# Performance work log

Hardware: AMD Instinct MI355X
Metric: run time of the kernel (lower is better)

## Reference

```python
import jax, jax.numpy as jnp
import numpy as np

NEG_SLOPE = 0.01  # torch F.leaky_relu default
NUM_USER, NUM_ITEM, DIM = 50000, 30000, 64
N_NODES = NUM_USER + NUM_ITEM
N_INTER = 800000
N_LAYERS = 2


def _leaky(x):
    return jax.nn.leaky_relu(x, NEG_SLOPE)


def _gcn_tower(features, preference, id_embedding, W, b, row, col):
    # x = cat(preference, features); F.normalize (L2 per row)
    x = jnp.concatenate([preference, features], axis=0)  # [N, 64]
    x = x / jnp.maximum(jnp.linalg.norm(x, axis=1, keepdims=True), 1e-12)
    deg = jax.ops.segment_sum(jnp.ones(row.shape, x.dtype), row, num_segments=N_NODES)  # bincount(row)
    for i in range(N_LAYERS):
        # Abstract_GCN: scatter-mean of gathered neighbor feats, then linear
        agg = jax.ops.segment_sum(x[col], row, num_segments=N_NODES) / deg[:, None]
        h = _leaky(agg @ W[i, 0].T + b[i, 0])
        # has_id=True, concate=False
        x_hat = _leaky(x @ W[i, 1].T + b[i, 1]) + id_embedding
        x = _leaky(h @ W[i, 2].T + b[i, 2] + x_hat)
    return x


def setup_inputs() -> dict:
    key = jax.random.key(0)
    ks = jax.random.split(key, 14)
    # bipartite user->item edges with full node coverage (every node appears
    # as a row after symmetrization, matching real interaction data where
    # bincount(row) has no zeros)
    r1 = jnp.arange(NUM_USER, dtype=jnp.int64 if jax.config.jax_enable_x64 else jnp.int32)
    c1 = jax.random.randint(ks[0], (NUM_USER,), NUM_USER, N_NODES)
    r2 = jax.random.randint(ks[1], (NUM_ITEM,), 0, NUM_USER)
    c2 = NUM_USER + jnp.arange(NUM_ITEM, dtype=r1.dtype)
    rest = N_INTER - NUM_USER - NUM_ITEM
    r3 = jax.random.randint(ks[2], (rest,), 0, NUM_USER)
    c3 = jax.random.randint(ks[3], (rest,), NUM_USER, N_NODES)
    row0 = jnp.concatenate([r1, r2, r3])
    col0 = jnp.concatenate([c1, c2, c3])
    # symmetrize: cat(edge_index, edge_index[[1,0]])
    edge_index = jnp.stack([jnp.concatenate([row0, col0]),
                            jnp.concatenate([col0, row0])])  # [2, 1.6M]
    s = 0.1  # xavier-ish scale for 64x64
    return {
        "v_feat": jax.random.normal(ks[4], (NUM_ITEM, DIM), jnp.float32),
        "t_feat": jax.random.normal(ks[5], (NUM_ITEM, DIM), jnp.float32),
        "id_embedding": jax.random.normal(ks[6], (N_NODES, DIM), jnp.float32) * s,
        "v_pref": jax.random.normal(ks[7], (NUM_USER, DIM), jnp.float32) * s,
        "t_pref": jax.random.normal(ks[8], (NUM_USER, DIM), jnp.float32) * s,
        "v_W": jax.random.normal(ks[9], (N_LAYERS, 3, DIM, DIM), jnp.float32) * s,
        "v_b": jnp.zeros((N_LAYERS, 3, DIM), jnp.float32),
        "t_W": jax.random.normal(ks[10], (N_LAYERS, 3, DIM, DIM), jnp.float32) * s,
        "t_b": jnp.zeros((N_LAYERS, 3, DIM), jnp.float32),
        "edge_index": edge_index,
    }


def reference(v_feat, t_feat, id_embedding, v_pref, t_pref, v_W, v_b, t_W, t_b, edge_index):
    row, col = edge_index[0], edge_index[1]
    rep_v = _gcn_tower(v_feat, v_pref, id_embedding, v_W, v_b, row, col)
    rep_t = _gcn_tower(t_feat, t_pref, id_embedding, t_W, t_b, row, col)
    return (rep_v + rep_t) / 2.0  # MMGCN.get_rep representation
```

## Files before the change

kernel.cpp:

```cpp
#include <hip/hip_runtime.h>
#include <hip/hip_bf16.h>

#define NUM_USER 50000
#define N_NODES  80000
#define DIM      64
#define NEG_SLOPE 0.01f

#define NB 313
#define BSHIFT 8
#define RMASK 255
#define CSHIFT 17
#define CMASK 0x1FFFF
#define CAP 10240

typedef __attribute__((ext_vector_type(8))) short short8;
typedef __attribute__((ext_vector_type(4))) float f32x4;

typedef unsigned short XT;

__device__ __forceinline__ float leaky(float v) {
    return v > 0.0f ? v : v * NEG_SLOPE;
}

__device__ __forceinline__ int load_idx(const void* ei, int is64, long long pos) {
    if (is64) return (int)((const long long*)ei)[pos];
    return ((const int*)ei)[pos];
}
__device__ __forceinline__ float load_f(const void* p, int isbf16, size_t i) {
    if (isbf16) return __bfloat162float(((const __hip_bfloat16*)p)[i]);
    return ((const float*)p)[i];
}

__device__ __forceinline__ unsigned short f2bf(float f) {
    unsigned u = __float_as_uint(f);
    u += 0x7fffu + ((u >> 16) & 1u);
    return (unsigned short)(u >> 16);
}

__device__ __forceinline__ void acc8(float* a, uint4 r) {
    a[0] += __uint_as_float(r.x << 16);
    a[1] += __uint_as_float(r.x & 0xffff0000u);
    a[2] += __uint_as_float(r.y << 16);
    a[3] += __uint_as_float(r.y & 0xffff0000u);
    a[4] += __uint_as_float(r.z << 16);
    a[5] += __uint_as_float(r.z & 0xffff0000u);
    a[6] += __uint_as_float(r.w << 16);
    a[7] += __uint_as_float(r.w & 0xffff0000u);
}

__global__ void detect_kernel(const unsigned int* __restrict__ feat_words,
                              const int* __restrict__ ei_words,
                              int* __restrict__ flags,
                              int* __restrict__ bucketCur) {
    int lane = threadIdx.x & 63;
    for (int i = lane; i < 320; i += 64) bucketCur[i] = 0;
    int orv = 0;
    for (int i = lane * 2 + 1; i < 1024; i += 128) orv |= ei_words[i];
    int hits = 0;
    for (int i = lane; i < 256; i += 64) {
        unsigned e = (feat_words[i] >> 7) & 0xFF;
        hits += (e == 126 || e == 127) ? 1 : 0;
    }
    #pragma unroll
    for (int d = 32; d > 0; d >>= 1) {
        orv  |= __shfl_xor(orv, d, 64);
        hits += __shfl_xor(hits, d, 64);
    }
    if (lane == 0 && blockIdx.x == 0) {
        flags[0] = (orv == 0) ? 1 : 0;
        flags[1] = (hits > 64) ? 1 : 0;
    }
}

__global__ __launch_bounds__(256) void megafuse_kernel(
        const void* __restrict__ ei, int E, int binBlocks, int initBlocks,
        const int* __restrict__ flags,
        int* __restrict__ bucketCur, unsigned int* __restrict__ recs,
        const void* __restrict__ vp, const void* __restrict__ tp,
        const void* __restrict__ vf, const void* __restrict__ tf,
        XT* __restrict__ xc,
        const void* __restrict__ vW, const void* __restrict__ tW,
        const void* __restrict__ vb, const void* __restrict__ tb,
        unsigned short* __restrict__ Wbf, float* __restrict__ bfp) {
    if ((int)blockIdx.x < binBlocks) {
        __shared__ int bloc[320];
        __shared__ int bres[320];
        int tid = threadIdx.x;
        for (int i = tid; i < 320; i += 256) bloc[i] = 0;
        __syncthreads();
        int is64 = flags[0];
        long long base = (long long)blockIdx.x * 2048;
        int bb[8], cc[8], lp[8], rl[8];
        #pragma unroll
        for (int it = 0; it < 8; ++it) {
            bb[it] = -1;
            long long e = base + it * 256 + tid;
            if (e < E) {
                int r = load_idx(ei, is64, e);
                int c = load_idx(ei, is64, (long long)E + e);
                if ((unsigned)r < N_NODES && (unsigned)c < N_NODES) {
                    int b = r >> BSHIFT;
                    bb[it] = b;
                    cc[it] = c;
                    rl[it] = r & RMASK;
                    lp[it] = atomicAdd(&bloc[b], 1);
                }
            }
        }
        __syncthreads();
        for (int i = tid; i < NB; i += 256) {
            int v = bloc[i];
            bres[i] = v ? atomicAdd(&bucketCur[i], v) : 0;
        }
        __syncthreads();
        #pragma unroll
        for (int it = 0; it < 8; ++it) {
            if (bb[it] >= 0) {
                int pos = bres[bb[it]] + lp[it];
                if (pos < CAP)
                    recs[(size_t)bb[it] * CAP + pos] =
                        ((unsigned)rl[it] << CSHIFT) | (unsigned)cc[it];
            }
        }
    } else if ((int)blockIdx.x < binBlocks + initBlocks) {
        int n = (blockIdx.x - binBlocks) * 4 + (threadIdx.x >> 6);
        if (n >= N_NODES) return;
        int lane = threadIdx.x & 63;
        int isb = flags[1];
        float a, b;
        if (n < NUM_USER) {
            a = load_f(vp, isb, (size_t)n * DIM + lane);
            b = load_f(tp, isb, (size_t)n * DIM + lane);
        } else {
            a = load_f(vf, isb, (size_t)(n - NUM_USER) * DIM + lane);
            b = load_f(tf, isb, (size_t)(n - NUM_USER) * DIM + lane);
        }
        float sa = a * a, sb = b * b;
        #pragma unroll
        for (int d = 32; d > 0; d >>= 1) {
            sa += __shfl_xor(sa, d, 64);
            sb += __shfl_xor(sb, d, 64);
        }
        float ra = 1.0f / fmaxf(sqrtf(sa), 1e-12f);
        float rb = 1.0f / fmaxf(sqrtf(sb), 1e-12f);
        xc[(size_t)n * 128 + lane]      = f2bf(a * ra);
        xc[(size_t)n * 128 + 64 + lane] = f2bf(b * rb);
    } else {
        int isb = flags[1];
        int j = (blockIdx.x - binBlocks - initBlocks) * 256 + threadIdx.x;
        if (j < 2 * 24576) {
            int tw = j / 24576, r = j % 24576;
            Wbf[j] = f2bf(load_f(tw ? tW : vW, isb, r));
        } else if (j < 2 * 24576 + 2 * 384) {
            int i2 = j - 2 * 24576;
            int tw = i2 / 384, r = i2 % 384;
            bfp[i2] = load_f(tw ? tb : vb, isb, r);
        }
    }
}

__global__ __launch_bounds__(1024) void bin2csr_kernel(
        const unsigned int* __restrict__ recs,
        const int* __restrict__ bucketCur,
        int* __restrict__ cnt, int* __restrict__ cur,
        int* __restrict__ csr) {
    __shared__ int rcnt[256];
    __shared__ int sc[256];
    __shared__ int lcur[256];
    int b = blockIdx.x;
    int t = threadIdx.x;
    int base = b * CAP;
    int count = bucketCur[b];
    if (count > CAP) count = CAP;

    if (t < 256) { rcnt[t] = 0; lcur[t] = 0; }
    __syncthreads();
    for (int i = t; i < count; i += 1024) {
        unsigned rec = recs[(size_t)base + i];
        atomicAdd(&rcnt[rec >> CSHIFT], 1);
    }
    __syncthreads();
    int v = (t < 256) ? rcnt[t] : 0;
    if (t < 256) sc[t] = v;
    __syncthreads();
    for (int d = 1; d < 256; d <<= 1) {
        int x = 0;
        if (t < 256) { x = sc[t]; if (t >= d) x += sc[t - d]; }
        __syncthreads();
        if (t < 256) sc[t] = x;
        __syncthreads();
    }
    if (t < 256) {
        int row = (b << BSHIFT) + t;
        if (row < N_NODES) {
            cnt[row] = v;
            cur[row] = base + sc[t];
        }
    }
    __syncthreads();
    for (int i = t; i < count; i += 1024) {
        unsigned rec = recs[(size_t)base + i];
        int rloc = rec >> CSHIFT;
        int c = rec & CMASK;
        int pos = base + (sc[rloc] - rcnt[rloc]) + atomicAdd(&lcur[rloc], 1);
        csr[pos] = c;
    }
}

__global__ __launch_bounds__(512) void gather_kernel(
        const XT* __restrict__ xc, XT* __restrict__ agg,
        const int* __restrict__ cnt, const int* __restrict__ cur,
        const int* __restrict__ csr) {
    int n = blockIdx.x * 8 + (threadIdx.x >> 6);
    if (n >= N_NODES) return;
    int lane = threadIdx.x & 63;
    int g8 = lane >> 3;
    int s  = lane & 7;
    int gg = g8 >> 1;
    int h  = g8 & 1;

    int d = cnt[n];
    int base = cur[n] - d;
    const int* nb = csr + base;
    const XT* xh = xc + h * 64;

    float acc[8];
    #pragma unroll
    for (int f = 0; f < 8; ++f) acc[f] = 0.f;

    int jj = gg;
    for (; jj + 4 < d; jj += 8) {
        int c0 = nb[jj];
        int c1 = nb[jj + 4];
        uint4 r0 = ((const uint4*)(xh + (size_t)c0 * 128))[s];
        uint4 r1 = ((const uint4*)(xh + (size_t)c1 * 128))[s];
        acc8(acc, r0);
        acc8(acc, r1);
    }
    if (jj < d) {
        int c0 = nb[jj];
        uint4 r0 = ((const uint4*)(xh + (size_t)c0 * 128))[s];
        acc8(acc, r0);
    }

    #pragma unroll
    for (int dd = 16; dd < 64; dd <<= 1) {
        #pragma unroll
        for (int f = 0; f < 8; ++f) acc[f] += __shfl_xor(acc[f], dd, 64);
    }

    float invd = (d > 0) ? 1.0f / (float)d : 0.0f;
    if (g8 < 2) {
        uint4 w;
        w.x = (unsigned)f2bf(acc[0] * invd) | ((unsigned)f2bf(acc[1] * invd) << 16);
        w.y = (unsigned)f2bf(acc[2] * invd) | ((unsigned)f2bf(acc[3] * invd) << 16);
        w.z = (unsigned)f2bf(acc[4] * invd) | ((unsigned)f2bf(acc[5] * invd) << 16);
        w.w = (unsigned)f2bf(acc[6] * invd) | ((unsigned)f2bf(acc[7] * invd) << 16);
        ((uint4*)(agg + (size_t)n * 128 + h * 64))[s] = w;
    }
}

__global__ __launch_bounds__(512) void dense_mfma_kernel(
        XT* __restrict__ xc, const XT* __restrict__ agg,
        const void* __restrict__ id_emb,
        const unsigned short* __restrict__ Wbf, const float* __restrict__ bfp,
        int layer, const int* __restrict__ flags) {
    __shared__ unsigned short Wl[3 * 64 * 72];
    __shared__ unsigned short hts[8][16 * 72];
    int tower = blockIdx.y;
    int wave = threadIdx.x >> 6, lane = threadIdx.x & 63;
    int quad = lane >> 4, l16 = lane & 15;
    int isb = flags[1];
    int toff = tower * 64;
    const unsigned short* Wg = Wbf + (size_t)((tower * 2 + layer) * 3) * 4096;
    const float* bb = bfp + (tower * 2 + layer) * 192;
    unsigned short* ht = hts[wave];

    for (int i = threadIdx.x; i < 1536; i += 512) {
        int lin = i * 8;
        int mat = lin >> 12;
        int rem = lin & 4095;
        uint4 v = *(const uint4*)(Wg + lin);
        *(uint4*)(Wl + mat * 4608 + (rem >> 6) * 72 + (rem & 63)) = v;
    }
    __syncthreads();

    int n0 = (blockIdx.x * 8 + wave) * 16;
    size_t arow = (size_t)(n0 + l16) * 128 + toff + quad * 8;

    short8 x0  = *(const short8*)(xc + arow);
    short8 x1  = *(const short8*)(xc + arow + 32);
    short8 ga0 = *(const short8*)(agg + arow);
    short8 ga1 = *(const short8*)(agg + arow + 32);

    f32x4 accP[4];

    #pragma unroll
    for (int t = 0; t < 4; ++t) {
        f32x4 c = {0.f, 0.f, 0.f, 0.f};
        short8 b0 = *(const short8*)(Wl + 4608 + (16 * t + l16) * 72 + quad * 8);
        short8 b1 = *(const short8*)(Wl + 4608 + (16 * t + l16) * 72 + 32 + quad * 8);
        c = __builtin_amdgcn_mfma_f32_16x16x32_bf16(x0, b0, c, 0, 0, 0);
        c = __builtin_amdgcn_mfma_f32_16x16x32_bf16(x1, b1, c, 0, 0, 0);
        float bias = bb[64 + 16 * t + l16];
        #pragma unroll
        for (int r = 0; r < 4; ++r) accP[t][r] = leaky(c[r] + bias);
    }

    #pragma unroll
    for (int t = 0; t < 4; ++t) {
        f32x4 c = {0.f, 0.f, 0.f, 0.f};
        short8 b0 = *(const short8*)(Wl + (16 * t + l16) * 72 + quad * 8);
        short8 b1 = *(const short8*)(Wl + (16 * t + l16) * 72 + 32 + quad * 8);
        c = __builtin_amdgcn_mfma_f32_16x16x32_bf16(ga0, b0, c, 0, 0, 0);
        c = __builtin_amdgcn_mfma_f32_16x16x32_bf16(ga1, b1, c, 0, 0, 0);
        float bias = bb[16 * t + l16];
        #pragma unroll
        for (int r = 0; r < 4; ++r)
            ht[(quad * 4 + r) * 72 + 16 * t + l16] = f2bf(leaky(c[r] + bias));
    }

    float idv[16];
    #pragma unroll
    for (int t = 0; t < 4; ++t)
        #pragma unroll
        for (int r = 0; r < 4; ++r)
            idv[t * 4 + r] = load_f(id_emb, isb,
                                    (size_t)(n0 + quad * 4 + r) * 64 + 16 * t + l16);

    short8 a0 = *(const short8*)(ht + l16 * 72 + quad * 8);
    short8 a1 = *(const short8*)(ht + l16 * 72 + 32 + quad * 8);

    #pragma unroll
    for (int t = 0; t < 4; ++t) {
        f32x4 c = {0.f, 0.f, 0.f, 0.f};
        short8 b0 = *(const short8*)(Wl + 2 * 4608 + (16 * t + l16) * 72 + quad * 8);
        short8 b1 = *(const short8*)(Wl + 2 * 4608 + (16 * t + l16) * 72 + 32 + quad * 8);
        c = __builtin_amdgcn_mfma_f32_16x16x32_bf16(a0, b0, c, 0, 0, 0);
        c = __builtin_amdgcn_mfma_f32_16x16x32_bf16(a1, b1, c, 0, 0, 0);
        float bias = bb[128 + 16 * t + l16];
        #pragma unroll
        for (int r = 0; r < 4; ++r) {
            int node2 = n0 + quad * 4 + r;
            int j = 16 * t + l16;
            float v = leaky(c[r] + bias + accP[t][r] + idv[t * 4 + r]);
            xc[(size_t)node2 * 128 + toff + j] = f2bf(v);
        }
    }
}

__global__ void final_kernel(const XT* __restrict__ xc, void* __restrict__ out,
                             const int* __restrict__ flags, int n8) {
    int i = blockIdx.x * blockDim.x + threadIdx.x;
    if (i >= n8) return;
    int n = i >> 3, s = i & 7;
    uint4 v = ((const uint4*)(xc + (size_t)n * 128))[s];
    uint4 t = ((const uint4*)(xc + (size_t)n * 128 + 64))[s];
    float r[8];
    r[0] = (__uint_as_float(v.x << 16) + __uint_as_float(t.x << 16)) * 0.5f;
    r[1] = (__uint_as_float(v.x & 0xffff0000u) + __uint_as_float(t.x & 0xffff0000u)) * 0.5f;
    r[2] = (__uint_as_float(v.y << 16) + __uint_as_float(t.y << 16)) * 0.5f;
    r[3] = (__uint_as_float(v.y & 0xffff0000u) + __uint_as_float(t.y & 0xffff0000u)) * 0.5f;
    r[4] = (__uint_as_float(v.z << 16) + __uint_as_float(t.z << 16)) * 0.5f;
    r[5] = (__uint_as_float(v.z & 0xffff0000u) + __uint_as_float(t.z & 0xffff0000u)) * 0.5f;
    r[6] = (__uint_as_float(v.w << 16) + __uint_as_float(t.w << 16)) * 0.5f;
    r[7] = (__uint_as_float(v.w & 0xffff0000u) + __uint_as_float(t.w & 0xffff0000u)) * 0.5f;
    if (flags[1]) {
        uint4 o;
        o.x = (unsigned)f2bf(r[0]) | ((unsigned)f2bf(r[1]) << 16);
        o.y = (unsigned)f2bf(r[2]) | ((unsigned)f2bf(r[3]) << 16);
        o.z = (unsigned)f2bf(r[4]) | ((unsigned)f2bf(r[5]) << 16);
        o.w = (unsigned)f2bf(r[6]) | ((unsigned)f2bf(r[7]) << 16);
        ((uint4*)out)[i] = o;
    } else {
        float4* o = (float4*)out;
        o[i * 2 + 0] = make_float4(r[0], r[1], r[2], r[3]);
        o[i * 2 + 1] = make_float4(r[4], r[5], r[6], r[7]);
    }
}

extern "C" void kernel_launch(void* const* d_in, const int* in_sizes, int n_in,
                              void* d_out, int out_size, void* d_ws, size_t ws_size,
                              hipStream_t stream) {
    const void* v_feat = d_in[0];
    const void* t_feat = d_in[1];
    const void* id_emb = d_in[2];
    const void* v_pref = d_in[3];
    const void* t_pref = d_in[4];
    const void* v_W    = d_in[5];
    const void* v_b    = d_in[6];
    const void* t_W    = d_in[7];
    const void* t_b    = d_in[8];
    const void* ei     = d_in[9];

    const int E = in_sizes[9] / 2;
    char* ws = (char*)d_ws;

    size_t o = 0;
    int*            flags     = (int*)(ws + o);            o += 16;
    int*            cnt       = (int*)(ws + o);            o += 320000;
    int*            cur       = (int*)(ws + o);            o += 320000;
    int*            bucketCur = (int*)(ws + o);            o += 320 * 4;
    unsigned short* Wbf       = (unsigned short*)(ws + o); o += 2 * 24576 * 2;
    float*          bfp       = (float*)(ws + o);          o += 2 * 384 * 4;
    XT* xc  = (XT*)(ws + o); o += (size_t)N_NODES * 128 * sizeof(XT);
    XT* agg = (XT*)(ws + o); o += (size_t)N_NODES * 128 * sizeof(XT);
    unsigned int* recs = (unsigned int*)(ws + o); o += (size_t)NB * CAP * 4;
    int* csr = (int*)(ws + o);

    detect_kernel<<<dim3(1), dim3(64), 0, stream>>>(
        (const unsigned int*)v_feat, (const int*)ei, flags, bucketCur);

    const int binBlocks  = (E + 2047) / 2048;
    const int initBlocks = (N_NODES + 3) / 4;
    const int packBlocks = (2 * 24576 + 2 * 384 + 255) / 256;
    megafuse_kernel<<<dim3(binBlocks + initBlocks + packBlocks), dim3(256), 0, stream>>>(
        ei, E, binBlocks, initBlocks, flags, bucketCur, recs,
        v_pref, t_pref, v_feat, t_feat, xc,
        v_W, t_W, v_b, t_b, Wbf, bfp);

    bin2csr_kernel<<<dim3(NB), dim3(1024), 0, stream>>>(recs, bucketCur, cnt, cur, csr);

    const int gatherBlocks = (N_NODES + 7) / 8;
    const int denseBlocksX = N_NODES / (16 * 8);

    for (int layer = 0; layer < 2; ++layer) {
        gather_kernel<<<dim3(gatherBlocks), dim3(512), 0, stream>>>(xc, agg, cnt, cur, csr);
        dense_mfma_kernel<<<dim3(denseBlocksX, 2), dim3(512), 0, stream>>>(
            xc, agg, id_emb, Wbf, bfp, layer, flags);
    }

    const int n8 = N_NODES * DIM / 8;
    final_kernel<<<dim3((n8 + 255) / 256), dim3(256), 0, stream>>>(xc, d_out, flags, n8);
}
```

Measured before the change: 344.6 us.

## Split interleaved tower feature buffers into separate per-tower arrays

After: 354.6 us. 2.9% more time.

```diff
diff --git a/kernel.cpp b/kernel.cpp
--- a/kernel.cpp
+++ b/kernel.cpp
@@ -78,7 +78,7 @@
         int* __restrict__ bucketCur, unsigned int* __restrict__ recs,
         const void* __restrict__ vp, const void* __restrict__ tp,
         const void* __restrict__ vf, const void* __restrict__ tf,
-        XT* __restrict__ xc,
+        XT* __restrict__ xv, XT* __restrict__ xt,
         const void* __restrict__ vW, const void* __restrict__ tW,
         const void* __restrict__ vb, const void* __restrict__ tb,
         unsigned short* __restrict__ Wbf, float* __restrict__ bfp) {
@@ -143,8 +143,8 @@
         }
         float ra = 1.0f / fmaxf(sqrtf(sa), 1e-12f);
         float rb = 1.0f / fmaxf(sqrtf(sb), 1e-12f);
-        xc[(size_t)n * 128 + lane]      = f2bf(a * ra);
-        xc[(size_t)n * 128 + 64 + lane] = f2bf(b * rb);
+        xv[(size_t)n * 64 + lane] = f2bf(a * ra);
+        xt[(size_t)n * 64 + lane] = f2bf(b * rb);
     } else {
         int isb = flags[1];
         int j = (blockIdx.x - binBlocks - initBlocks) * 256 + threadIdx.x;
@@ -208,70 +208,73 @@
 }
 
 __global__ __launch_bounds__(512) void gather_kernel(
-        const XT* __restrict__ xc, XT* __restrict__ agg,
+        const XT* __restrict__ xv, const XT* __restrict__ xt,
+        XT* __restrict__ aggv, XT* __restrict__ aggt,
         const int* __restrict__ cnt, const int* __restrict__ cur,
         const int* __restrict__ csr) {
     int n = blockIdx.x * 8 + (threadIdx.x >> 6);
     if (n >= N_NODES) return;
+    int tower = blockIdx.y;
+    const XT* xh = tower ? xt : xv;
+    XT* ah = tower ? aggt : aggv;
     int lane = threadIdx.x & 63;
-    int g8 = lane >> 3;
-    int s  = lane & 7;
-    int gg = g8 >> 1;
-    int h  = g8 & 1;
+    int g = lane >> 3;
+    int s = lane & 7;
 
     int d = cnt[n];
     int base = cur[n] - d;
     const int* nb = csr + base;
-    const XT* xh = xc + h * 64;
 
     float acc[8];
     #pragma unroll
     for (int f = 0; f < 8; ++f) acc[f] = 0.f;
 
-    int jj = gg;
-    for (; jj + 4 < d; jj += 8) {
+    int jj = g;
+    for (; jj + 8 < d; jj += 16) {
         int c0 = nb[jj];
-        int c1 = nb[jj + 4];
-        uint4 r0 = ((const uint4*)(xh + (size_t)c0 * 128))[s];
-        uint4 r1 = ((const uint4*)(xh + (size_t)c1 * 128))[s];
+        int c1 = nb[jj + 8];
+        uint4 r0 = ((const uint4*)(xh + (size_t)c0 * 64))[s];
+        uint4 r1 = ((const uint4*)(xh + (size_t)c1 * 64))[s];
         acc8(acc, r0);
         acc8(acc, r1);
     }
     if (jj < d) {
         int c0 = nb[jj];
-        uint4 r0 = ((const uint4*)(xh + (size_t)c0 * 128))[s];
+        uint4 r0 = ((const uint4*)(xh + (size_t)c0 * 64))[s];
         acc8(acc, r0);
     }
 
     #pragma unroll
-    for (int dd = 16; dd < 64; dd <<= 1) {
+    for (int dd = 8; dd < 64; dd <<= 1) {
         #pragma unroll
         for (int f = 0; f < 8; ++f) acc[f] += __shfl_xor(acc[f], dd, 64);
     }
 
     float invd = (d > 0) ? 1.0f / (float)d : 0.0f;
-    if (g8 < 2) {
+    if (g == 0) {
         uint4 w;
         w.x = (unsigned)f2bf(acc[0] * invd) | ((unsigned)f2bf(acc[1] * invd) << 16);
         w.y = (unsigned)f2bf(acc[2] * invd) | ((unsigned)f2bf(acc[3] * invd) << 16);
         w.z = (unsigned)f2bf(acc[4] * invd) | ((unsigned)f2bf(acc[5] * invd) << 16);
         w.w = (unsigned)f2bf(acc[6] * invd) | ((unsigned)f2bf(acc[7] * invd) << 16);
-        ((uint4*)(agg + (size_t)n * 128 + h * 64))[s] = w;
+        ((uint4*)(ah + (size_t)n * 64))[s] = w;
     }
 }
 
 __global__ __launch_bounds__(512) void dense_mfma_kernel(
-        XT* __restrict__ xc, const XT* __restrict__ agg,
+        XT* __restrict__ xv, XT* __restrict__ xt,
+        const XT* __restrict__ aggv, const XT* __restrict__ aggt,
         const void* __restrict__ id_emb,
         const unsigned short* __restrict__ Wbf, const float* __restrict__ bfp,
         int layer, const int* __restrict__ flags) {
     __shared__ unsigned short Wl[3 * 64 * 72];
     __shared__ unsigned short hts[8][16 * 72];
     int tower = blockIdx.y;
+    XT* xh = tower ? xt : xv;
+    const XT* ah = tower ? aggt : aggv;
     int wave = threadIdx.x >> 6, lane = threadIdx.x & 63;
     int quad = lane >> 4, l16 = lane & 15;
     int isb = flags[1];
-    int toff = tower * 64;
     const unsigned short* Wg = Wbf + (size_t)((tower * 2 + layer) * 3) * 4096;
     const float* bb = bfp + (tower * 2 + layer) * 192;
     unsigned short* ht = hts[wave];
@@ -286,12 +289,12 @@
     __syncthreads();
 
     int n0 = (blockIdx.x * 8 + wave) * 16;
-    size_t arow = (size_t)(n0 + l16) * 128 + toff + quad * 8;
-
-    short8 x0  = *(const short8*)(xc + arow);
-    short8 x1  = *(const short8*)(xc + arow + 32);
-    short8 ga0 = *(const short8*)(agg + arow);
-    short8 ga1 = *(const short8*)(agg + arow + 32);
+    size_t arow = (size_t)(n0 + l16) * 64 + quad * 8;
+
+    short8 x0  = *(const short8*)(xh + arow);
+    short8 x1  = *(const short8*)(xh + arow + 32);
+    short8 ga0 = *(const short8*)(ah + arow);
+    short8 ga1 = *(const short8*)(ah + arow + 32);
 
     f32x4 accP[4];
 
@@ -344,18 +347,18 @@
             int node2 = n0 + quad * 4 + r;
             int j = 16 * t + l16;
             float v = leaky(c[r] + bias + accP[t][r] + idv[t * 4 + r]);
-            xc[(size_t)node2 * 128 + toff + j] = f2bf(v);
-        }
-    }
-}
-
-__global__ void final_kernel(const XT* __restrict__ xc, void* __restrict__ out,
+            xh[(size_t)node2 * 64 + j] = f2bf(v);
+        }
+    }
+}
+
+__global__ void final_kernel(const XT* __restrict__ xv, const XT* __restrict__ xt,
+                             void* __restrict__ out,
                              const int* __restrict__ flags, int n8) {
     int i = blockIdx.x * blockDim.x + threadIdx.x;
     if (i >= n8) return;
-    int n = i >> 3, s = i & 7;
-    uint4 v = ((const uint4*)(xc + (size_t)n * 128))[s];
-    uint4 t = ((const uint4*)(xc + (size_t)n * 128 + 64))[s];
+    uint4 v = ((const uint4*)xv)[i];
+    uint4 t = ((const uint4*)xt)[i];
     float r[8];
     r[0] = (__uint_as_float(v.x << 16) + __uint_as_float(t.x << 16)) * 0.5f;
     r[1] = (__uint_as_float(v.x & 0xffff0000u) + __uint_as_float(t.x & 0xffff0000u)) * 0.5f;
@@ -403,8 +406,10 @@
     int*            bucketCur = (int*)(ws + o);            o += 320 * 4;
     unsigned short* Wbf       = (unsigned short*)(ws + o); o += 2 * 24576 * 2;
     float*          bfp       = (float*)(ws + o);          o += 2 * 384 * 4;
-    XT* xc  = (XT*)(ws + o); o += (size_t)N_NODES * 128 * sizeof(XT);
-    XT* agg = (XT*)(ws + o); o += (size_t)N_NODES * 128 * sizeof(XT);
+    XT* xv   = (XT*)(ws + o); o += (size_t)N_NODES * 64 * sizeof(XT);
+    XT* xt   = (XT*)(ws + o); o += (size_t)N_NODES * 64 * sizeof(XT);
+    XT* aggv = (XT*)(ws + o); o += (size_t)N_NODES * 64 * sizeof(XT);
+    XT* aggt = (XT*)(ws + o); o += (size_t)N_NODES * 64 * sizeof(XT);
     unsigned int* recs = (unsigned int*)(ws + o); o += (size_t)NB * CAP * 4;
     int* csr = (int*)(ws + o);
 
@@ -416,7 +421,7 @@
     const int packBlocks = (2 * 24576 + 2 * 384 + 255) / 256;
     megafuse_kernel<<<dim3(binBlocks + initBlocks + packBlocks), dim3(256), 0, stream>>>(
         ei, E, binBlocks, initBlocks, flags, bucketCur, recs,
-        v_pref, t_pref, v_feat, t_feat, xc,
+        v_pref, t_pref, v_feat, t_feat, xv, xt,
         v_W, t_W, v_b, t_b, Wbf, bfp);
 
     bin2csr_kernel<<<dim3(NB), dim3(1024), 0, stream>>>(recs, bucketCur, cnt, cur, csr);
@@ -425,11 +430,13 @@
     const int denseBlocksX = N_NODES / (16 * 8);
 
     for (int layer = 0; layer < 2; ++layer) {
-        gather_kernel<<<dim3(gatherBlocks), dim3(512), 0, stream>>>(xc, agg, cnt, cur, csr);
+        gather_kernel<<<dim3(gatherBlocks, 2), dim3(512), 0, stream>>>(
+            xv, xt, aggv, aggt, cnt, cur, csr);
         dense_mfma_kernel<<<dim3(denseBlocksX, 2), dim3(512), 0, stream>>>(
-            xc, agg, id_emb, Wbf, bfp, layer, flags);
+            xv, xt, aggv, aggt, id_emb, Wbf, bfp, layer, flags);
     }
 
     const int n8 = N_NODES * DIM / 8;
-    final_kernel<<<dim3((n8 + 255) / 256), dim3(256), 0, stream>>>(xc, d_out, flags, n8);
-}
+    final_kernel<<<dim3((n8 + 255) / 256), dim3(256), 0, stream>>>(
+        xv, xt, d_out, flags, n8);
+}
```

## Two-pass edge binning with larger blocks and nontemporal loads in gather

Applied to the files above, without the earlier changes.

Result: slower. 368.2 us (+6.9%).

```diff
diff --git a/kernel.cpp b/kernel.cpp
--- a/kernel.cpp
+++ b/kernel.cpp
@@ -15,6 +15,7 @@
 
 typedef __attribute__((ext_vector_type(8))) short short8;
 typedef __attribute__((ext_vector_type(4))) float f32x4;
+typedef __attribute__((ext_vector_type(4))) unsigned int u32x4;
 
 typedef unsigned short XT;
 
@@ -89,37 +90,34 @@
         for (int i = tid; i < 320; i += 256) bloc[i] = 0;
         __syncthreads();
         int is64 = flags[0];
-        long long base = (long long)blockIdx.x * 2048;
-        int bb[8], cc[8], lp[8], rl[8];
-        #pragma unroll
-        for (int it = 0; it < 8; ++it) {
-            bb[it] = -1;
+        long long base = (long long)blockIdx.x * 8192;
+        for (int it = 0; it < 32; ++it) {
+            long long e = base + it * 256 + tid;
+            if (e < E) {
+                int r = load_idx(ei, is64, e);
+                int c = load_idx(ei, is64, (long long)E + e);
+                if ((unsigned)r < N_NODES && (unsigned)c < N_NODES)
+                    atomicAdd(&bloc[r >> BSHIFT], 1);
+            }
+        }
+        __syncthreads();
+        for (int i = tid; i < NB; i += 256) {
+            int v = bloc[i];
+            bres[i] = v ? atomicAdd(&bucketCur[i], v) : 0;
+        }
+        __syncthreads();
+        for (int it = 0; it < 32; ++it) {
             long long e = base + it * 256 + tid;
             if (e < E) {
                 int r = load_idx(ei, is64, e);
                 int c = load_idx(ei, is64, (long long)E + e);
                 if ((unsigned)r < N_NODES && (unsigned)c < N_NODES) {
                     int b = r >> BSHIFT;
-                    bb[it] = b;
-                    cc[it] = c;
-                    rl[it] = r & RMASK;
-                    lp[it] = atomicAdd(&bloc[b], 1);
+                    int pos = atomicAdd(&bres[b], 1);
+                    if (pos < CAP)
+                        recs[(size_t)b * CAP + pos] =
+                            ((unsigned)(r & RMASK) << CSHIFT) | (unsigned)c;
                 }
-            }
-        }
-        __syncthreads();
-        for (int i = tid; i < NB; i += 256) {
-            int v = bloc[i];
-            bres[i] = v ? atomicAdd(&bucketCur[i], v) : 0;
-        }
-        __syncthreads();
-        #pragma unroll
-        for (int it = 0; it < 8; ++it) {
-            if (bb[it] >= 0) {
-                int pos = bres[bb[it]] + lp[it];
-                if (pos < CAP)
-                    recs[(size_t)bb[it] * CAP + pos] =
-                        ((unsigned)rl[it] << CSHIFT) | (unsigned)cc[it];
             }
         }
     } else if ((int)blockIdx.x < binBlocks + initBlocks) {
@@ -219,8 +217,8 @@
     int gg = g8 >> 1;
     int h  = g8 & 1;
 
-    int d = cnt[n];
-    int base = cur[n] - d;
+    int d = __builtin_nontemporal_load(cnt + n);
+    int base = __builtin_nontemporal_load(cur + n) - d;
     const int* nb = csr + base;
     const XT* xh = xc + h * 64;
 
@@ -230,15 +228,15 @@
 
     int jj = gg;
     for (; jj + 4 < d; jj += 8) {
-        int c0 = nb[jj];
-        int c1 = nb[jj + 4];
+        int c0 = __builtin_nontemporal_load(nb + jj);
+        int c1 = __builtin_nontemporal_load(nb + jj + 4);
         uint4 r0 = ((const uint4*)(xh + (size_t)c0 * 128))[s];
         uint4 r1 = ((const uint4*)(xh + (size_t)c1 * 128))[s];
         acc8(acc, r0);
         acc8(acc, r1);
     }
     if (jj < d) {
-        int c0 = nb[jj];
+        int c0 = __builtin_nontemporal_load(nb + jj);
         uint4 r0 = ((const uint4*)(xh + (size_t)c0 * 128))[s];
         acc8(acc, r0);
     }
@@ -251,12 +249,12 @@
 
     float invd = (d > 0) ? 1.0f / (float)d : 0.0f;
     if (g8 < 2) {
-        uint4 w;
+        u32x4 w;
         w.x = (unsigned)f2bf(acc[0] * invd) | ((unsigned)f2bf(acc[1] * invd) << 16);
         w.y = (unsigned)f2bf(acc[2] * invd) | ((unsigned)f2bf(acc[3] * invd) << 16);
         w.z = (unsigned)f2bf(acc[4] * invd) | ((unsigned)f2bf(acc[5] * invd) << 16);
         w.w = (unsigned)f2bf(acc[6] * invd) | ((unsigned)f2bf(acc[7] * invd) << 16);
-        ((uint4*)(agg + (size_t)n * 128 + h * 64))[s] = w;
+        __builtin_nontemporal_store(w, (u32x4*)(agg + (size_t)n * 128 + h * 64) + s);
     }
 }
 
@@ -411,7 +409,7 @@
     detect_kernel<<<dim3(1), dim3(64), 0, stream>>>(
         (const unsigned int*)v_feat, (const int*)ei, flags, bucketCur);
 
-    const int binBlocks  = (E + 2047) / 2048;
+    const int binBlocks  = (E + 8191) / 8192;
     const int initBlocks = (N_NODES + 3) / 4;
     const int packBlocks = (2 * 24576 + 2 * 384 + 255) / 256;
     megafuse_kernel<<<dim3(binBlocks + initBlocks + packBlocks), dim3(256), 0, stream>>>(
```
